# Performance work log

Hardware: AMD Instinct MI355X
Metric: run time of the kernel (lower is better)

Reference implementation:

```python
import jax, jax.numpy as jnp
import numpy as np

B, LA, LB, D = 16, 1024, 1024, 1024

def setup_inputs() -> dict:
    key = jax.random.key(0)
    k1, k2 = jax.random.split(key)
    premise_encoded = jax.random.normal(k1, (B, LA, D), dtype=jnp.float32)
    hypothesis_encoded = jax.random.normal(k2, (B, LB, D), dtype=jnp.float32)
    return {"premise_encoded": premise_encoded, "hypothesis_encoded": hypothesis_encoded}

def reference(premise_encoded, hypothesis_encoded):
    # L2-normalize along feature dim (cosine similarity scores)
    p_norm = premise_encoded / jnp.linalg.norm(premise_encoded, axis=2, keepdims=True)
    h_norm = hypothesis_encoded / jnp.linalg.norm(hypothesis_encoded, axis=2, keepdims=True)
    # eij: [B, La, Lb]
    eij = jnp.einsum('bad,bhd->bah', p_norm, h_norm)
    # row-softmax over hypothesis positions -> attend hypothesis for each premise token
    a_tilde = jnp.einsum('bah,bhd->bad', jax.nn.softmax(eij, axis=-1), hypothesis_encoded)
    # column direction: softmax of eij^T over premise positions -> attend premise
    b_tilde = jnp.einsum('bha,bad->bhd', jax.nn.softmax(jnp.swapaxes(eij, 1, 2), axis=-1), premise_encoded)
    return (a_tilde, b_tilde)
```

## Files before the change

### kernel.cpp

```cpp
#include <hip/hip_runtime.h>
#include <stdint.h>

#define BATCH 16
#define SEQ   1024
#define DIM   1024

static const size_t NE = (size_t)BATCH * SEQ * DIM;

typedef short short8 __attribute__((ext_vector_type(8)));
typedef float f32x4  __attribute__((ext_vector_type(4)));

typedef __attribute__((address_space(1))) const unsigned int g_u32;
typedef __attribute__((address_space(3))) unsigned int l_u32;

__device__ __forceinline__ float bf2f(unsigned short u) {
  return __uint_as_float(((unsigned int)u) << 16);
}
__device__ __forceinline__ unsigned short f2bf(float f) {
  unsigned int u = __float_as_uint(f);
  u += 0x7FFFu + ((u >> 16) & 1u);
  return (unsigned short)(u >> 16);
}
__device__ __forceinline__ void gl_lds16(const unsigned short* g, unsigned short* l) {
  __builtin_amdgcn_global_load_lds((g_u32*)g, (l_u32*)l, 16, 0, 0);
}

__global__ __launch_bounds__(256) void k_cvt(
    const float* __restrict__ P, const float* __restrict__ Hp,
    unsigned short* __restrict__ P16, unsigned short* __restrict__ H16,
    unsigned short* __restrict__ P16T, unsigned short* __restrict__ H16T,
    float* __restrict__ invP, float* __restrict__ invH)
{
  const int b  = blockIdx.x;
  const int rb = blockIdx.y;
  const float* src; unsigned short* dst; unsigned short* dstT; float* inv;
  if (blockIdx.z == 0) { src = P;  dst = P16; dstT = P16T; inv = invP; }
  else                 { src = Hp; dst = H16; dstT = H16T; inv = invH; }
  src  += (size_t)b*SEQ*DIM + (size_t)rb*64*DIM;
  dst  += (size_t)b*SEQ*DIM + (size_t)rb*64*DIM;
  dstT += (size_t)b*SEQ*DIM + (size_t)rb*64;
  inv  += b*SEQ + rb*64;

  __shared__ unsigned short Ls[64*65];
  __shared__ float rowacc[64];
  const int t = threadIdx.x;
  if (t < 64) rowacc[t] = 0.f;
  __syncthreads();

  for (int ct = 0; ct < 16; ++ct) {
    #pragma unroll
    for (int round = 0; round < 4; ++round) {
      int idx = round*256 + t;
      int r = idx >> 4;
      int c = (idx & 15) * 4;
      float4 x = *(const float4*)(src + (size_t)r*DIM + ct*64 + c);
      float ss = x.x*x.x + x.y*x.y + x.z*x.z + x.w*x.w;
      ss += __shfl_xor(ss, 1);
      ss += __shfl_xor(ss, 2);
      ss += __shfl_xor(ss, 4);
      ss += __shfl_xor(ss, 8);
      if ((t & 15) == 0) rowacc[r] += ss;
      unsigned short h0=f2bf(x.x), h1=f2bf(x.y), h2=f2bf(x.z), h3=f2bf(x.w);
      union { unsigned short us[4]; uint2 u; } pk;
      pk.us[0]=h0; pk.us[1]=h1; pk.us[2]=h2; pk.us[3]=h3;
      *(uint2*)(dst + (size_t)r*DIM + ct*64 + c) = pk.u;
      Ls[r*65 + c + 0] = h0;
      Ls[r*65 + c + 1] = h1;
      Ls[r*65 + c + 2] = h2;
      Ls[r*65 + c + 3] = h3;
    }
    __syncthreads();
    {
      int dloc = t >> 2;
      int a0   = (t & 3) * 16;
      union { unsigned short us[16]; uint4 u[2]; } pk;
      #pragma unroll
      for (int jj = 0; jj < 16; ++jj) pk.us[jj] = Ls[(a0+jj)*65 + dloc];
      unsigned short* o = dstT + (size_t)(ct*64 + dloc)*SEQ + a0;
      *(uint4*)(o)     = pk.u[0];
      *(uint4*)(o + 8) = pk.u[1];
    }
    __syncthreads();
  }
  if (t < 64) inv[t] = rsqrtf(rowacc[t]);
}

template<int MODE>
__global__ __launch_bounds__(256) void k_gemm(
    const unsigned short* __restrict__ A,
    const unsigned short* __restrict__ Bm,
    void* __restrict__ Cout,
    const float* __restrict__ sRow,
    const float* __restrict__ sCol)
{
  __shared__ unsigned short As[128*32];
  __shared__ unsigned short Bs[128*32];
  const int b    = blockIdx.x;
  const int brow = blockIdx.y * 128;
  const int bcol = blockIdx.z * 128;
  const int t = threadIdx.x;
  const int w = t >> 6, l = t & 63;
  const int wr = w >> 1, wc = w & 1;

  const size_t boff = (size_t)b << 20;
  const unsigned short* gA0 = A  + boff + (size_t)(brow + w*32 + (l>>2))*DIM + (l&3)*8;
  const unsigned short* gB0 = Bm + boff + (size_t)(bcol + w*32 + (l>>2))*DIM + (l&3)*8;
  unsigned short* lA0 = &As[(w*2+0)*512];
  unsigned short* lA1 = &As[(w*2+1)*512];
  unsigned short* lB0 = &Bs[(w*2+0)*512];
  unsigned short* lB1 = &Bs[(w*2+1)*512];

  f32x4 acc[4][4];
  #pragma unroll
  for (int m = 0; m < 4; ++m)
    #pragma unroll
    for (int n = 0; n < 4; ++n)
      acc[m][n] = (f32x4){0.f,0.f,0.f,0.f};

  const int fr = l & 15;
  const int kg = (l >> 4) * 8;

  for (int kt = 0; kt < 32; ++kt) {
    const int k0 = kt * 32;
    gl_lds16(gA0 + k0,          lA0);
    gl_lds16(gA0 + 16*DIM + k0, lA1);
    gl_lds16(gB0 + k0,          lB0);
    gl_lds16(gB0 + 16*DIM + k0, lB1);
    __syncthreads();
    short8 af[4], bf[4];
    #pragma unroll
    for (int m = 0; m < 4; ++m)
      af[m] = *(const short8*)&As[(wr*64 + m*16 + fr)*32 + kg];
    #pragma unroll
    for (int n = 0; n < 4; ++n)
      bf[n] = *(const short8*)&Bs[(wc*64 + n*16 + fr)*32 + kg];
    #pragma unroll
    for (int m = 0; m < 4; ++m)
      #pragma unroll
      for (int n = 0; n < 4; ++n)
        acc[m][n] = __builtin_amdgcn_mfma_f32_16x16x32_bf16(af[m], bf[n], acc[m][n], 0, 0, 0);
    __syncthreads();
  }

  const int rb0 = brow + wr*64 + ((l>>4)<<2);
  const int cb0 = bcol + wc*64 + fr;
  if (MODE == 0) {
    unsigned short* E = (unsigned short*)Cout + boff;
    #pragma unroll
    for (int n = 0; n < 4; ++n) {
      const int c = cb0 + n*16;
      const float ic = sCol[b*SEQ + c];
      #pragma unroll
      for (int m = 0; m < 4; ++m) {
        const int r0 = rb0 + m*16;
        #pragma unroll
        for (int j = 0; j < 4; ++j) {
          float s = acc[m][n][j] * sRow[b*SEQ + r0 + j] * ic;
          E[(size_t)(r0 + j)*SEQ + c] = f2bf(__expf(s));
        }
      }
    }
  } else {
    float* C = (float*)Cout + boff;
    #pragma unroll
    for (int n = 0; n < 4; ++n) {
      const int c = cb0 + n*16;
      #pragma unroll
      for (int m = 0; m < 4; ++m) {
        const int r0 = rb0 + m*16;
        #pragma unroll
        for (int j = 0; j < 4; ++j)
          C[(size_t)(r0 + j)*SEQ + c] = acc[m][n][j] * sRow[b*SEQ + r0 + j];
      }
    }
  }
}

__global__ __launch_bounds__(256) void k_rowinv(
    const unsigned short* __restrict__ E, float* __restrict__ out)
{
  const int row = blockIdx.x*4 + (threadIdx.x >> 6);
  const int l = threadIdx.x & 63;
  const unsigned short* p = E + (size_t)row*SEQ + l*8;
  float s = 0.f;
  #pragma unroll
  for (int h = 0; h < 2; ++h) {
    union { uint4 u; unsigned short us[8]; } d;
    d.u = *(const uint4*)(p + h*512);
    #pragma unroll
    for (int j = 0; j < 8; ++j) s += bf2f(d.us[j]);
  }
  #pragma unroll
  for (int off = 1; off < 64; off <<= 1) s += __shfl_xor(s, off);
  if (l == 0) out[row] = 1.0f / s;
}

extern "C" void kernel_launch(void* const* d_in, const int* in_sizes, int n_in,
                              void* d_out, int out_size, void* d_ws, size_t ws_size,
                              hipStream_t stream)
{
  const float* P  = (const float*)d_in[0];
  const float* Hp = (const float*)d_in[1];
  float* outF = (float*)d_out;
  float* aOut = outF;
  float* bOut = outF + NE;

  unsigned short* P16  = (unsigned short*)d_ws;
  unsigned short* H16  = P16  + NE;
  unsigned short* P16T = H16  + NE;
  unsigned short* H16T = P16T + NE;
  if (ws_size < 4 * NE * sizeof(unsigned short)) return;

  unsigned short* E = (unsigned short*)bOut;
  float* smalls = bOut + NE/2;
  float* invP  = smalls;
  float* invH  = smalls + BATCH*SEQ;
  float* raInv = smalls + 2*BATCH*SEQ;
  float* rbInv = (float*)P16;

  dim3 blk(256);
  dim3 gg(BATCH, 8, 8);

  k_cvt<<<dim3(BATCH,16,2), blk, 0, stream>>>(P, Hp, P16, H16, P16T, H16T, invP, invH);
  k_gemm<0><<<gg, blk, 0, stream>>>(P16, H16, (void*)E, invP, invH);
  k_rowinv<<<dim3(BATCH*SEQ/4), blk, 0, stream>>>(E, raInv);
  k_gemm<1><<<gg, blk, 0, stream>>>(E, H16T, (void*)aOut, raInv, nullptr);
  k_gemm<0><<<gg, blk, 0, stream>>>(H16, P16, (void*)H16T, invH, invP);
  k_rowinv<<<dim3(BATCH*SEQ/4), blk, 0, stream>>>(H16T, rbInv);
  k_gemm<1><<<gg, blk, 0, stream>>>(H16T, P16T, (void*)bOut, rbInv, nullptr);
}
```

Baseline: 485.4 us.

## Enlarge GEMM tiles to 256x256 with double-buffered LDS and split conversion kernel

The GEMM moves from 128x128 tiles with 256 threads and a single 32-wide K buffer to 256x256 tiles with 512 threads, a 64-wide K step, and two LDS buffers, so the next tile's loads overlap the current MFMA work. The conversion kernel is split four ways along the feature dimension for more parallelism, with row sums accumulated atomically and a separate kernel applying rsqrt. The larger tiles cut global reload traffic but use 128KB of LDS and 128 accumulator registers per thread, which limits occupancy, and the grid shrinks to 256 blocks.

Measured after the change: 502.9 us. 1.04x slower.

```diff
diff --git a/kernel.cpp b/kernel.cpp
--- a/kernel.cpp
+++ b/kernel.cpp
@@ -6,6 +6,7 @@
 #define DIM   1024
 
 static const size_t NE = (size_t)BATCH * SEQ * DIM;
+static const int    BS = BATCH * SEQ;
 
 typedef short short8 __attribute__((ext_vector_type(8)));
 typedef float f32x4  __attribute__((ext_vector_type(4)));
@@ -29,17 +30,18 @@
     const float* __restrict__ P, const float* __restrict__ Hp,
     unsigned short* __restrict__ P16, unsigned short* __restrict__ H16,
     unsigned short* __restrict__ P16T, unsigned short* __restrict__ H16T,
-    float* __restrict__ invP, float* __restrict__ invH)
-{
-  const int b  = blockIdx.x;
-  const int rb = blockIdx.y;
-  const float* src; unsigned short* dst; unsigned short* dstT; float* inv;
-  if (blockIdx.z == 0) { src = P;  dst = P16; dstT = P16T; inv = invP; }
-  else                 { src = Hp; dst = H16; dstT = H16T; inv = invH; }
+    float* __restrict__ accP, float* __restrict__ accH)
+{
+  const int b   = blockIdx.x;
+  const int rb  = blockIdx.y >> 2;
+  const int ctg = blockIdx.y & 3;
+  const float* src; unsigned short* dst; unsigned short* dstT; float* acc;
+  if (blockIdx.z == 0) { src = P;  dst = P16; dstT = P16T; acc = accP; }
+  else                 { src = Hp; dst = H16; dstT = H16T; acc = accH; }
   src  += (size_t)b*SEQ*DIM + (size_t)rb*64*DIM;
   dst  += (size_t)b*SEQ*DIM + (size_t)rb*64*DIM;
   dstT += (size_t)b*SEQ*DIM + (size_t)rb*64;
-  inv  += b*SEQ + rb*64;
+  acc  += b*SEQ + rb*64;
 
   __shared__ unsigned short Ls[64*65];
   __shared__ float rowacc[64];
@@ -47,7 +49,7 @@
   if (t < 64) rowacc[t] = 0.f;
   __syncthreads();
 
-  for (int ct = 0; ct < 16; ++ct) {
+  for (int ct = ctg*4; ct < ctg*4 + 4; ++ct) {
     #pragma unroll
     for (int round = 0; round < 4; ++round) {
       int idx = round*256 + t;
@@ -82,81 +84,103 @@
     }
     __syncthreads();
   }
-  if (t < 64) inv[t] = rsqrtf(rowacc[t]);
+  if (t < 64) atomicAdd(&acc[t], rowacc[t]);
+}
+
+__global__ __launch_bounds__(256) void k_norm(
+    const float* __restrict__ accP, const float* __restrict__ accH,
+    float* __restrict__ invP, float* __restrict__ invH)
+{
+  const int i = blockIdx.x*256 + threadIdx.x;
+  if (i < BS) invP[i] = rsqrtf(accP[i]);
+  else        invH[i - BS] = rsqrtf(accH[i - BS]);
 }
 
 template<int MODE>
-__global__ __launch_bounds__(256) void k_gemm(
+__global__ __launch_bounds__(512, 2) void k_gemm(
     const unsigned short* __restrict__ A,
     const unsigned short* __restrict__ Bm,
     void* __restrict__ Cout,
     const float* __restrict__ sRow,
     const float* __restrict__ sCol)
 {
-  __shared__ unsigned short As[128*32];
-  __shared__ unsigned short Bs[128*32];
-  const int b    = blockIdx.x;
-  const int brow = blockIdx.y * 128;
-  const int bcol = blockIdx.z * 128;
+  __shared__ unsigned short smA[2][256*64];
+  __shared__ unsigned short smB[2][256*64];
+  const int b    = blockIdx.z;
+  const int brow = blockIdx.y * 256;
+  const int bcol = blockIdx.x * 256;
   const int t = threadIdx.x;
   const int w = t >> 6, l = t & 63;
-  const int wr = w >> 1, wc = w & 1;
+  const int wr = w >> 2, wc = w & 3;
 
   const size_t boff = (size_t)b << 20;
-  const unsigned short* gA0 = A  + boff + (size_t)(brow + w*32 + (l>>2))*DIM + (l&3)*8;
-  const unsigned short* gB0 = Bm + boff + (size_t)(bcol + w*32 + (l>>2))*DIM + (l&3)*8;
-  unsigned short* lA0 = &As[(w*2+0)*512];
-  unsigned short* lA1 = &As[(w*2+1)*512];
-  unsigned short* lB0 = &Bs[(w*2+0)*512];
-  unsigned short* lB1 = &Bs[(w*2+1)*512];
-
-  f32x4 acc[4][4];
+  const unsigned short* gAt = A  + boff + (size_t)(brow + w*8 + (l>>3))*DIM + (l&7)*8;
+  const unsigned short* gBt = Bm + boff + (size_t)(bcol + w*8 + (l>>3))*DIM + (l&7)*8;
+
+  f32x4 acc[8][4];
   #pragma unroll
-  for (int m = 0; m < 4; ++m)
+  for (int m = 0; m < 8; ++m)
     #pragma unroll
     for (int n = 0; n < 4; ++n)
       acc[m][n] = (f32x4){0.f,0.f,0.f,0.f};
 
-  const int fr = l & 15;
-  const int kg = (l >> 4) * 8;
-
-  for (int kt = 0; kt < 32; ++kt) {
-    const int k0 = kt * 32;
-    gl_lds16(gA0 + k0,          lA0);
-    gl_lds16(gA0 + 16*DIM + k0, lA1);
-    gl_lds16(gB0 + k0,          lB0);
-    gl_lds16(gB0 + 16*DIM + k0, lB1);
+  const int frow = l & 15;
+  const int kg8  = (l >> 4) * 8;
+  const int aofs = (wr*128 + frow)*64 + kg8;
+  const int bofs = (wc*64  + frow)*64 + kg8;
+
+  #define STAGE(BUF, K0) do {                                          \
+    const unsigned short* ga_ = gAt + (K0);                            \
+    const unsigned short* gb_ = gBt + (K0);                            \
+    unsigned short* la_ = &smA[(BUF)][w*8*64];  \
+    unsigned short* lb_ = &smB[(BUF)][w*8*64];                         \
+    _Pragma("unroll")                                                  \
+    for (int r_ = 0; r_ < 4; ++r_) {                                   \
+      gl_lds16(ga_ + (size_t)r_*64*DIM, la_ + r_*4096);                \
+      gl_lds16(gb_ + (size_t)r_*64*DIM, lb_ + r_*4096);                \
+    }                                                                  \
+  } while (0)
+
+  STAGE(0, 0);
+  __syncthreads();
+  int cur = 0;
+  for (int kt = 0; kt < 16; ++kt) {
+    if (kt < 15) STAGE(cur ^ 1, (kt+1)*64);
+    #pragma unroll
+    for (int ks = 0; ks < 2; ++ks) {
+      short8 af[8], bf[4];
+      #pragma unroll
+      for (int m = 0; m < 8; ++m)
+        af[m] = *(const short8*)&smA[cur][aofs + m*1024 + ks*32];
+      #pragma unroll
+      for (int n = 0; n < 4; ++n)
+        bf[n] = *(const short8*)&smB[cur][bofs + n*1024 + ks*32];
+      #pragma unroll
+      for (int m = 0; m < 8; ++m)
+        #pragma unroll
+        for (int n = 0; n < 4; ++n)
+          acc[m][n] = __builtin_amdgcn_mfma_f32_16x16x32_bf16(af[m], bf[n], acc[m][n], 0, 0, 0);
+    }
     __syncthreads();
-    short8 af[4], bf[4];
-    #pragma unroll
-    for (int m = 0; m < 4; ++m)
-      af[m] = *(const short8*)&As[(wr*64 + m*16 + fr)*32 + kg];
-    #pragma unroll
-    for (int n = 0; n < 4; ++n)
-      bf[n] = *(const short8*)&Bs[(wc*64 + n*16 + fr)*32 + kg];
-    #pragma unroll
-    for (int m = 0; m < 4; ++m)
-      #pragma unroll
-      for (int n = 0; n < 4; ++n)
-        acc[m][n] = __builtin_amdgcn_mfma_f32_16x16x32_bf16(af[m], bf[n], acc[m][n], 0, 0, 0);
-    __syncthreads();
-  }
-
-  const int rb0 = brow + wr*64 + ((l>>4)<<2);
-  const int cb0 = bcol + wc*64 + fr;
+    cur ^= 1;
+  }
+  #undef STAGE
+
+  const int r0l = wr*128 + ((l>>4)<<2);
+  const int c0l = wc*64 + frow;
   if (MODE == 0) {
     unsigned short* E = (unsigned short*)Cout + boff;
     #pragma unroll
     for (int n = 0; n < 4; ++n) {
-      const int c = cb0 + n*16;
+      const int c = bcol + c0l + n*16;
       const float ic = sCol[b*SEQ + c];
       #pragma unroll
-      for (int m = 0; m < 4; ++m) {
-        const int r0 = rb0 + m*16;
+      for (int m = 0; m < 8; ++m) {
         #pragma unroll
         for (int j = 0; j < 4; ++j) {
-          float s = acc[m][n][j] * sRow[b*SEQ + r0 + j] * ic;
-          E[(size_t)(r0 + j)*SEQ + c] = f2bf(__expf(s));
+          const int r = brow + r0l + m*16 + j;
+          float s = acc[m][n][j] * sRow[b*SEQ + r] * ic;
+          E[(size_t)r*SEQ + c] = f2bf(__expf(s));
         }
       }
     }
@@ -164,13 +188,14 @@
     float* C = (float*)Cout + boff;
     #pragma unroll
     for (int n = 0; n < 4; ++n) {
-      const int c = cb0 + n*16;
-      #pragma unroll
-      for (int m = 0; m < 4; ++m) {
-        const int r0 = rb0 + m*16;
+      const int c = bcol + c0l + n*16;
+      #pragma unroll
+      for (int m = 0; m < 8; ++m) {
         #pragma unroll
-        for (int j = 0; j < 4; ++j)
-          C[(size_t)(r0 + j)*SEQ + c] = acc[m][n][j] * sRow[b*SEQ + r0 + j];
+        for (int j = 0; j < 4; ++j) {
+          const int r = brow + r0l + m*16 + j;
+          C[(size_t)r*SEQ + c] = acc[m][n][j] * sRow[b*SEQ + r];
+        }
       }
     }
   }
@@ -214,18 +239,19 @@
   unsigned short* E = (unsigned short*)bOut;
   float* smalls = bOut + NE/2;
   float* invP  = smalls;
-  float* invH  = smalls + BATCH*SEQ;
-  float* raInv = smalls + 2*BATCH*SEQ;
+  float* invH  = smalls + BS;
+  float* raInv = smalls + 2*BS;
+  float* accP  = smalls + 3*BS;
+  float* accH  = smalls + 4*BS;
   float* rbInv = (float*)P16;
 
-  dim3 blk(256);
-  dim3 gg(BATCH, 8, 8);
-
-  k_cvt<<<dim3(BATCH,16,2), blk, 0, stream>>>(P, Hp, P16, H16, P16T, H16T, invP, invH);
-  k_gemm<0><<<gg, blk, 0, stream>>>(P16, H16, (void*)E, invP, invH);
-  k_rowinv<<<dim3(BATCH*SEQ/4), blk, 0, stream>>>(E, raInv);
-  k_gemm<1><<<gg, blk, 0, stream>>>(E, H16T, (void*)aOut, raInv, nullptr);
-  k_gemm<0><<<gg, blk, 0, stream>>>(H16, P16, (void*)H16T, invH, invP);
-  k_rowinv<<<dim3(BATCH*SEQ/4), blk, 0, stream>>>(H16T, rbInv);
-  k_gemm<1><<<gg, blk, 0, stream>>>(H16T, P16T, (void*)bOut, rbInv, nullptr);
-}
+  hipMemsetAsync(accP, 0, 2*(size_t)BS*sizeof(float), stream);
+  k_cvt<<<dim3(BATCH,64,2), 256, 0, stream>>>(P, Hp, P16, H16, P16T, H16T, accP, accH);
+  k_norm<<<dim3(2*BS/256), 256, 0, stream>>>(accP, accH, invP, invH);
+  k_gemm<0><<<dim3(4,4,BATCH), 512, 0, stream>>>(P16, H16, (void*)E, invP, invH);
+  k_rowinv<<<dim3(BS/4), 256, 0, stream>>>(E, raInv);
+  k_gemm<1><<<dim3(4,4,BATCH), 512, 0, stream>>>(E, H16T, (void*)aOut, raInv, nullptr);
+  k_gemm<0><<<dim3(4,4,BATCH), 512, 0, stream>>>(H16, P16, (void*)H16T, invH, invP);
+  k_rowinv<<<dim3(BS/4), 256, 0, stream>>>(H16T, rbInv);
+  k_gemm<1><<<dim3(4,4,BATCH), 512, 0, stream>>>(H16T, P16T, (void*)bOut, rbInv, nullptr);
+}
```
